# Optimization experiments

Measured on AMD Instinct MI355X. Metric: run time of the kernel, lower is better.

Reference implementation:

```python
import jax, jax.numpy as jnp
import numpy as np

B, LT, LI, DT, DI, D, H = 128, 96, 64, 1024, 2048, 1024, 4
NEG = -2.0 ** 31  # tf.pow(-2.0, 31)
EPS = 1e-3        # keras LayerNormalization default epsilon


def _mha(q_in, k_in, v_in, q_mask, k_mask, Wq, Wk, Wv, Wo):
    # tf split-heads: chunk i of axis 2 -> head i; reshape (B,L,H,d) matches.
    d = D // H
    b = q_in.shape[0]
    q = (q_in @ Wq).reshape(b, -1, H, d)
    k = (k_in @ Wk).reshape(b, -1, H, d)
    v = (v_in @ Wv).reshape(b, -1, H, d)
    scores = jnp.einsum('bqhd,bkhd->bhqk', q, k) / jnp.sqrt(jnp.float32(d))
    mask = (q_mask != 0)[:, None, :, None] & (k_mask != 0)[:, None, None, :]  # [B,1,Lq,Lk]
    scores = jnp.where(mask, scores, NEG)
    attn = jax.nn.softmax(scores, axis=-1)
    attn = jnp.where(mask, attn, 0.0)  # dropout rate is 0.0 -> identity
    out = jnp.einsum('bhqk,bkhd->bqhd', attn, v).reshape(b, -1, D)
    return out @ Wo


def _ln(x, g, b):
    m = jnp.mean(x, axis=-1, keepdims=True)
    v = jnp.var(x, axis=-1, keepdims=True)
    return (x - m) / jnp.sqrt(v + EPS) * g + b


def setup_inputs() -> dict:
    key = jax.random.key(0)
    ks = iter(jax.random.split(key, 40))
    s = 0.02
    inp = {
        'text_embedding': jax.random.normal(next(ks), (B, LT, DT), jnp.float32),
        'image_embedding': jax.random.normal(next(ks), (B, LI, DI), jnp.float32),
        'text_mask': jax.random.randint(next(ks), (B, LT), 0, 2, jnp.int32),
        'image_mask': jax.random.randint(next(ks), (B, LI), 0, 2, jnp.int32),
        'W_tp': jax.random.normal(next(ks), (DT, D), jnp.float32) * s,
        'b_tp': jnp.zeros((D,), jnp.float32),
        'W_ip': jax.random.normal(next(ks), (DI, D), jnp.float32) * s,
        'b_ip': jnp.zeros((D,), jnp.float32),
        # text cross-attn (query=image_proj, key=text_proj, value=RAW text)
        'ta_Wq': jax.random.normal(next(ks), (D, D), jnp.float32) * s,
        'ta_Wk': jax.random.normal(next(ks), (D, D), jnp.float32) * s,
        'ta_Wv': jax.random.normal(next(ks), (DT, D), jnp.float32) * s,
        'ta_Wo': jax.random.normal(next(ks), (D, D), jnp.float32) * s,
        # image cross-attn (query=text_proj, key=image_proj, value=RAW image)
        'ia_Wq': jax.random.normal(next(ks), (D, D), jnp.float32) * s,
        'ia_Wk': jax.random.normal(next(ks), (D, D), jnp.float32) * s,
        'ia_Wv': jax.random.normal(next(ks), (DI, D), jnp.float32) * s,
        'ia_Wo': jax.random.normal(next(ks), (D, D), jnp.float32) * s,
        # self-attention blocks
        'ts_Wq': jax.random.normal(next(ks), (D, D), jnp.float32) * s,
        'ts_Wk': jax.random.normal(next(ks), (D, D), jnp.float32) * s,
        'ts_Wv': jax.random.normal(next(ks), (D, D), jnp.float32) * s,
        'ts_Wo': jax.random.normal(next(ks), (D, D), jnp.float32) * s,
        'is_Wq': jax.random.normal(next(ks), (D, D), jnp.float32) * s,
        'is_Wk': jax.random.normal(next(ks), (D, D), jnp.float32) * s,
        'is_Wv': jax.random.normal(next(ks), (D, D), jnp.float32) * s,
        'is_Wo': jax.random.normal(next(ks), (D, D), jnp.float32) * s,
        # layernorm params
        'ln_ta_g': jnp.ones((D,), jnp.float32), 'ln_ta_b': jnp.zeros((D,), jnp.float32),
        'ln_ia_g': jnp.ones((D,), jnp.float32), 'ln_ia_b': jnp.zeros((D,), jnp.float32),
        'ln_ts_g': jnp.ones((D,), jnp.float32), 'ln_ts_b': jnp.zeros((D,), jnp.float32),
        'ln_is_g': jnp.ones((D,), jnp.float32), 'ln_is_b': jnp.zeros((D,), jnp.float32),
    }
    return inp


def reference(text_embedding, image_embedding, text_mask, image_mask,
              W_tp, b_tp, W_ip, b_ip,
              ta_Wq, ta_Wk, ta_Wv, ta_Wo,
              ia_Wq, ia_Wk, ia_Wv, ia_Wo,
              ts_Wq, ts_Wk, ts_Wv, ts_Wo,
              is_Wq, is_Wk, is_Wv, is_Wo,
              ln_ta_g, ln_ta_b, ln_ia_g, ln_ia_b,
              ln_ts_g, ln_ts_b, ln_is_g, ln_is_b):
    text_proj = text_embedding @ W_tp + b_tp    # [B,LT,D]
    image_proj = image_embedding @ W_ip + b_ip  # [B,LI,D]
    # cross attention (note asymmetric query/key masks, raw-value inputs)
    text_att = _mha(image_proj, text_proj, text_embedding, image_mask, text_mask,
                    ta_Wq, ta_Wk, ta_Wv, ta_Wo)   # [B,LI,D]
    image_att = _mha(text_proj, image_proj, image_embedding, text_mask, image_mask,
                     ia_Wq, ia_Wk, ia_Wv, ia_Wo)  # [B,LT,D]
    text_att = _ln(text_att, ln_ta_g, ln_ta_b)
    image_att = _ln(image_att, ln_ia_g, ln_ia_b)
    # self attention
    text_att = _mha(text_att, text_att, text_att, image_mask, image_mask,
                    ts_Wq, ts_Wk, ts_Wv, ts_Wo)
    image_att = _mha(image_att, image_att, image_att, text_mask, text_mask,
                     is_Wq, is_Wk, is_Wv, is_Wo)
    text_att = _ln(text_att, ln_ts_g, ln_ts_b)
    image_att = _ln(image_att, ln_is_g, ln_is_b)
    return (text_att, image_att)
```

## Files before the change

### kernel.cpp

```cpp
#include <hip/hip_runtime.h>

typedef __bf16 bf16_t;
typedef __attribute__((ext_vector_type(8))) __bf16 bf16x8;
typedef __attribute__((ext_vector_type(4))) __bf16 bf16x4;
typedef __attribute__((ext_vector_type(4))) float f32x4;

__device__ __forceinline__ void async_copy16(const bf16_t* g, bf16_t* l) {
    __builtin_amdgcn_global_load_lds(
        (const __attribute__((address_space(1))) void*)g,
        (__attribute__((address_space(3))) void*)l, 16, 0, 0);
}

__global__ __launch_bounds__(256) void cvt_bf16(const float* __restrict__ in,
                                                bf16_t* __restrict__ out) {
    int i = (blockIdx.x * 256 + threadIdx.x) * 4;
    float4 v = *(const float4*)(in + i);
    bf16x4 o;
    o[0] = (__bf16)v.x; o[1] = (__bf16)v.y; o[2] = (__bf16)v.z; o[3] = (__bf16)v.w;
    *(bf16x4*)(out + i) = o;
}

__global__ __launch_bounds__(256) void transpose_group(const float* __restrict__ s0,
                                                       const float* __restrict__ s1,
                                                       const float* __restrict__ s2,
                                                       bf16_t* __restrict__ dst, int K) {
    const float* in;
    if (blockIdx.z == 0) in = s0;
    else if (blockIdx.z == 1) in = s1;
    else in = s2;
    bf16_t* out = dst + (size_t)blockIdx.z * 1024 * K;
    __shared__ float tile[32][33];
    int t = threadIdx.x;
    int tx = t & 31, ty = t >> 5;
    int n0 = blockIdx.x * 32, k0 = blockIdx.y * 32;
#pragma unroll
    for (int i = 0; i < 4; i++) {
        int k = k0 + ty + i * 8;
        tile[ty + i * 8][tx] = in[(size_t)k * 1024 + n0 + tx];
    }
    __syncthreads();
#pragma unroll
    for (int i = 0; i < 4; i++) {
        int n = n0 + ty + i * 8;
        out[(size_t)n * K + k0 + tx] = (bf16_t)tile[tx][ty + i * 8];
    }
}

__global__ __launch_bounds__(256) void fuse_bias(const float* __restrict__ src,
                                                 float* __restrict__ out) {
    int i = blockIdx.x * 256 + threadIdx.x;
    out[i] = (i < 1024) ? src[i] : 0.f;
}

__global__ __launch_bounds__(512, 2) void gemm256(const bf16_t* __restrict__ A,
                                                  const bf16_t* __restrict__ Bt,
                                                  const float* __restrict__ bias,
                                                  bf16_t* __restrict__ o0,
                                                  bf16_t* __restrict__ o1,
                                                  bf16_t* __restrict__ o2,
                                                  int M, int N, int K) {
    (void)M; (void)N;
    __shared__ bf16_t Ls[65536];
    const int t = threadIdx.x;
    const int w = t >> 6, lane = t & 63;
    const int l16 = lane & 15, quad = lane >> 4;
    const int wm2 = w >> 2, wn4 = w & 3;

    const int nx = gridDim.x;
    const int nwg = nx * gridDim.y;
    const int flat = blockIdx.y * nx + blockIdx.x;
    const int chunk = nwg >> 3;
    const int swz = (flat & 7) * chunk + (flat >> 3);
    const int bm = (swz % nx) * 256;
    const int bn = (swz / nx) * 256;

    const int NT = K >> 5;

    const int sl = t & 7;
    const int pl = (t >> 3) & 63;
    const int ss = sl ^ (pl & 7);
    const int srow = (pl << 1) | (ss >> 2);
    const int scol = (ss & 3) << 3;
    const bf16_t* gA = A + (size_t)(bm + srow) * K + scol;
    const bf16_t* gB = Bt + (size_t)(bn + srow) * K + scol;
    const size_t rstep = (size_t)128 * K;
    const int ldW = w * 512;

    int offA[8], offB[4];
#pragma unroll
    for (int mf = 0; mf < 8; mf++) {
        int row = wm2 * 128 + mf * 16 + l16;
        int p = row >> 1;
        int s2 = (((row & 1) << 2) | quad) ^ (p & 7);
        offA[mf] = p * 64 + s2 * 8;
    }
#pragma unroll
    for (int nf = 0; nf < 4; nf++) {
        int row = wn4 * 64 + nf * 16 + l16;
        int p = row >> 1;
        int s2 = (((row & 1) << 2) | quad) ^ (p & 7);
        offB[nf] = 8192 + p * 64 + s2 * 8;
    }

    const f32x4 zero = {0.f, 0.f, 0.f, 0.f};
    f32x4 acc[8][4];
#pragma unroll
    for (int i = 0; i < 8; i++)
#pragma unroll
        for (int j = 0; j < 4; j++) acc[i][j] = zero;

#pragma unroll
    for (int pt = 0; pt < 3; pt++) {
        bf16_t* lb = Ls + pt * 16384 + ldW;
        const bf16_t* a0 = gA + pt * 32;
        const bf16_t* b0 = gB + pt * 32;
        async_copy16(a0, lb);
        async_copy16(a0 + rstep, lb + 4096);
        async_copy16(b0, lb + 8192);
        async_copy16(b0 + rstep, lb + 12288);
    }
    asm volatile("s_waitcnt vmcnt(8)" ::: "memory");
    __builtin_amdgcn_s_barrier();
    __builtin_amdgcn_sched_barrier(0);

    for (int t0 = 0; t0 < NT; t0++) {
        const bf16_t* cb = Ls + (t0 & 3) * 16384;
        bf16_t* sb = Ls + ((t0 + 3) & 3) * 16384 + ldW;
        const bf16_t* ga = gA + (size_t)(t0 + 3) * 32;
        const bf16_t* gb = gB + (size_t)(t0 + 3) * 32;
        const bool st = (t0 + 3 < NT);
        bf16x8 bq[4], aq[4], ar[4];

#pragma unroll
        for (int nf = 0; nf < 4; nf++) bq[nf] = *(const bf16x8*)(cb + offB[nf]);
#pragma unroll
        for (int mf = 0; mf < 4; mf++) aq[mf] = *(const bf16x8*)(cb + offA[mf]);
        if (st) {
            async_copy16(ga, sb);
            async_copy16(ga + rstep, sb + 4096);
        }
        __builtin_amdgcn_s_barrier();
        __builtin_amdgcn_s_setprio(1);
#pragma unroll
        for (int mf = 0; mf < 4; mf++)
#pragma unroll
            for (int nf = 0; nf < 4; nf++)
                acc[mf][nf] = __builtin_amdgcn_mfma_f32_16x16x32_bf16(aq[mf], bq[nf], acc[mf][nf], 0, 0, 0);
        __builtin_amdgcn_s_setprio(0);
        __builtin_amdgcn_s_barrier();

#pragma unroll
        for (int mf = 0; mf < 4; mf++) ar[mf] = *(const bf16x8*)(cb + offA[4 + mf]);
        if (st) {
            async_copy16(gb, sb + 8192);
            async_copy16(gb + rstep, sb + 12288);
        }
        __builtin_amdgcn_s_barrier();
        __builtin_amdgcn_s_setprio(1);
#pragma unroll
        for (int mf = 0; mf < 4; mf++)
#pragma unroll
            for (int nf = 0; nf < 4; nf++)
                acc[4 + mf][nf] = __builtin_amdgcn_mfma_f32_16x16x32_bf16(ar[mf], bq[nf], acc[4 + mf][nf], 0, 0, 0);
        __builtin_amdgcn_s_setprio(0);

        if (t0 + 1 < NT) {
            if (t0 + 3 < NT)      asm volatile("s_waitcnt vmcnt(8)" ::: "memory");
            else if (t0 + 2 < NT) asm volatile("s_waitcnt vmcnt(4)" ::: "memory");
            else                  asm volatile("s_waitcnt vmcnt(0)" ::: "memory");
            __builtin_amdgcn_s_barrier();
            __builtin_amdgcn_sched_barrier(0);
        }
    }

    bf16_t* outp;
    if (bn < 1024) outp = o0;
    else if (bn < 2048) outp = o1;
    else outp = o2;
    const int cseg = bn & 1023;
    float bsv[4];
#pragma unroll
    for (int nf = 0; nf < 4; nf++)
        bsv[nf] = bias ? bias[bn + wn4 * 64 + nf * 16 + l16] : 0.f;
#pragma unroll
    for (int mf = 0; mf < 8; mf++) {
        int r0 = bm + wm2 * 128 + mf * 16 + quad * 4;
#pragma unroll
        for (int nf = 0; nf < 4; nf++) {
            int c = cseg + wn4 * 64 + nf * 16 + l16;
#pragma unroll
            for (int r = 0; r < 4; r++)
                outp[(size_t)(r0 + r) * 1024 + c] = (bf16_t)(acc[mf][nf][r] + bsv[nf]);
        }
    }
}

template <int LQ, int LK>
__global__ __launch_bounds__(256) void attn_kernel(const bf16_t* __restrict__ Q,
                                                   const bf16_t* __restrict__ Kb,
                                                   const bf16_t* __restrict__ V,
                                                   const int* __restrict__ qmask,
                                                   const int* __restrict__ kmask,
                                                   bf16_t* __restrict__ O) {
    constexpr int VSTR = LK + 8;
    constexpr int NQT = LQ / 16, NKT = LK / 16, NKB = LK / 32;
    __shared__ bf16_t Vt[256 * VSTR];
    __shared__ bf16_t Pb[4 * 16 * LK];

    const int t = threadIdx.x;
    const int w = t >> 6, lane = t & 63;
    const int quad = lane >> 4, l16 = lane & 15;
    const int b = blockIdx.x >> 2;
    const int h = blockIdx.x & 3;
    const int hoff = h * 256;

    for (int idx = t; idx < LK * 32; idx += 256) {
        int k = idx % LK;
        int e0 = (idx / LK) * 8;
        bf16x8 v = *(const bf16x8*)(V + (size_t)(b * LK + k) * 1024 + hoff + e0);
#pragma unroll
        for (int j = 0; j < 8; j++) Vt[(e0 + j) * VSTR + k] = v[j];
    }
    __syncthreads();

    bf16_t* P = Pb + w * (16 * LK);

    for (int qt = w; qt < NQT; qt += 4) {
        const int qrow = b * LQ + qt * 16;
        bf16x8 qf[8];
#pragma unroll
        for (int kb = 0; kb < 8; kb++)
            qf[kb] = *(const bf16x8*)(Q + (size_t)(qrow + l16) * 1024 + hoff + kb * 32 + quad * 8);

        f32x4 s[NKT];
        const f32x4 zero = {0.f, 0.f, 0.f, 0.f};
#pragma unroll
        for (int nt = 0; nt < NKT; nt++) {
            f32x4 a = zero;
#pragma unroll
            for (int kb = 0; kb < 8; kb++) {
                bf16x8 kf = *(const bf16x8*)(Kb + (size_t)(b * LK + nt * 16 + l16) * 1024 + hoff + kb * 32 + quad * 8);
                a = __builtin_amdgcn_mfma_f32_16x16x32_bf16(qf[kb], kf, a, 0, 0, 0);
            }
            s[nt] = a;
        }

        int km[NKT];
#pragma unroll
        for (int nt = 0; nt < NKT; nt++) km[nt] = kmask[b * LK + nt * 16 + l16];
        int qmv[4];
#pragma unroll
        for (int r = 0; r < 4; r++) qmv[r] = qmask[b * LQ + qt * 16 + quad * 4 + r];

        float rmax[4], rsum[4];
#pragma unroll
        for (int r = 0; r < 4; r++) rmax[r] = -3.0e38f;
#pragma unroll
        for (int nt = 0; nt < NKT; nt++)
#pragma unroll
            for (int r = 0; r < 4; r++) {
                float v = s[nt][r] * 0.0625f;
                bool ok = (qmv[r] != 0) && (km[nt] != 0);
                s[nt][r] = ok ? v : -3.0e38f;
                rmax[r] = fmaxf(rmax[r], s[nt][r]);
            }
#pragma unroll
        for (int r = 0; r < 4; r++)
            for (int off = 1; off < 16; off <<= 1)
                rmax[r] = fmaxf(rmax[r], __shfl_xor(rmax[r], off, 16));
#pragma unroll
        for (int r = 0; r < 4; r++) rsum[r] = 0.f;
#pragma unroll
        for (int nt = 0; nt < NKT; nt++)
#pragma unroll
            for (int r = 0; r < 4; r++) {
                float p = (s[nt][r] > -1.0e38f) ? __expf(s[nt][r] - rmax[r]) : 0.f;
                s[nt][r] = p;
                rsum[r] += p;
            }
#pragma unroll
        for (int r = 0; r < 4; r++)
            for (int off = 1; off < 16; off <<= 1)
                rsum[r] += __shfl_xor(rsum[r], off, 16);
#pragma unroll
        for (int r = 0; r < 4; r++) rsum[r] = (rsum[r] > 0.f) ? 1.f / rsum[r] : 0.f;

#pragma unroll
        for (int nt = 0; nt < NKT; nt++)
#pragma unroll
            for (int r = 0; r < 4; r++)
                P[(quad * 4 + r) * LK + nt * 16 + l16] = (bf16_t)(s[nt][r] * rsum[r]);
        asm volatile("s_waitcnt lgkmcnt(0)" ::: "memory");

        bf16x8 pf[NKB];
#pragma unroll
        for (int kb = 0; kb < NKB; kb++)
            pf[kb] = *(const bf16x8*)(P + l16 * LK + kb * 32 + quad * 8);

#pragma unroll
        for (int et = 0; et < 16; et++) {
            f32x4 o = zero;
#pragma unroll
            for (int kb = 0; kb < NKB; kb++) {
                bf16x8 vf = *(const bf16x8*)(Vt + (et * 16 + l16) * VSTR + kb * 32 + quad * 8);
                o = __builtin_amdgcn_mfma_f32_16x16x32_bf16(pf[kb], vf, o, 0, 0, 0);
            }
#pragma unroll
            for (int r = 0; r < 4; r++)
                O[(size_t)(qrow + quad * 4 + r) * 1024 + hoff + et * 16 + l16] = (bf16_t)o[r];
        }
    }
}

__global__ __launch_bounds__(256) void ln_kernel(const bf16_t* __restrict__ in,
                                                 const float* __restrict__ g,
                                                 const float* __restrict__ be,
                                                 float* __restrict__ outF,
                                                 bf16_t* __restrict__ outB) {
    __shared__ float red[8];
    const int row = blockIdx.x, t = threadIdx.x;
    bf16x4 xb = *(const bf16x4*)(in + (size_t)row * 1024 + t * 4);
    float x0 = (float)xb[0], x1 = (float)xb[1], x2 = (float)xb[2], x3 = (float)xb[3];
    float s = x0 + x1 + x2 + x3;
    float ss = x0 * x0 + x1 * x1 + x2 * x2 + x3 * x3;
    for (int off = 1; off < 64; off <<= 1) {
        s += __shfl_xor(s, off);
        ss += __shfl_xor(ss, off);
    }
    int w = t >> 6, lane = t & 63;
    if (lane == 0) { red[w * 2] = s; red[w * 2 + 1] = ss; }
    __syncthreads();
    if (t == 0) {
        float a = 0.f, b2 = 0.f;
        for (int i = 0; i < 4; i++) { a += red[i * 2]; b2 += red[i * 2 + 1]; }
        red[0] = a; red[1] = b2;
    }
    __syncthreads();
    float mean = red[0] * (1.f / 1024.f);
    float var = red[1] * (1.f / 1024.f) - mean * mean;
    float rstd = rsqrtf(var + 1e-3f);
    float4 gv = *(const float4*)(g + t * 4);
    float4 bv = *(const float4*)(be + t * 4);
    float y0 = (x0 - mean) * rstd * gv.x + bv.x;
    float y1 = (x1 - mean) * rstd * gv.y + bv.y;
    float y2 = (x2 - mean) * rstd * gv.z + bv.z;
    float y3 = (x3 - mean) * rstd * gv.w + bv.w;
    if (outF) {
        float4 o = {y0, y1, y2, y3};
        *(float4*)(outF + (size_t)row * 1024 + t * 4) = o;
    }
    if (outB) {
        bf16x4 o;
        o[0] = (__bf16)y0; o[1] = (__bf16)y1; o[2] = (__bf16)y2; o[3] = (__bf16)y3;
        *(bf16x4*)(outB + (size_t)row * 1024 + t * 4) = o;
    }
}

extern "C" void kernel_launch(void* const* d_in, const int* in_sizes, int n_in,
                              void* d_out, int out_size, void* d_ws, size_t ws_size,
                              hipStream_t stream) {
    (void)in_sizes; (void)n_in; (void)out_size; (void)ws_size;
    const float* tE = (const float*)d_in[0];
    const float* iE = (const float*)d_in[1];
    const int* tMask = (const int*)d_in[2];
    const int* iMask = (const int*)d_in[3];

    const size_t MB = 1048576;
    char* ws = (char*)d_ws;
    bf16_t* WB = (bf16_t*)ws;
    float* biasT = (float*)(ws + 8 * MB);
    float* biasI = biasT + 2048;
    char* AB = ws + 9 * MB;
    auto buf = [&](int mb) { return (bf16_t*)(AB + (size_t)mb * MB); };

    auto TG = [&](int i0, int i1, int i2, int parts, int K) {
        transpose_group<<<dim3(32, K / 32, parts), 256, 0, stream>>>(
            (const float*)d_in[i0], i1 >= 0 ? (const float*)d_in[i1] : (const float*)d_in[i0],
            i2 >= 0 ? (const float*)d_in[i2] : (const float*)d_in[i0], WB, K);
    };
    auto gemm = [&](const bf16_t* A, const float* bias, bf16_t* out0, bf16_t* out1,
                    bf16_t* out2, int M, int N, int K) {
        gemm256<<<dim3(M / 256, N / 256), 512, 0, stream>>>(A, WB, bias, out0, out1, out2, M, N, K);
    };

    fuse_bias<<<8, 256, 0, stream>>>((const float*)d_in[5], biasT);
    fuse_bias<<<8, 256, 0, stream>>>((const float*)d_in[7], biasI);

    cvt_bf16<<<12288, 256, 0, stream>>>(tE, buf(88));
    TG(4, 10, -1, 2, 1024);
    gemm(buf(88), biasT, buf(32), buf(64), nullptr, 12288, 2048, 1024);
    cvt_bf16<<<16384, 256, 0, stream>>>(iE, buf(88));
    TG(6, 14, -1, 2, 2048);
    gemm(buf(88), biasI, buf(0), buf(16), nullptr, 8192, 2048, 2048);
    TG(9, 12, -1, 2, 1024);
    gemm(buf(32), nullptr, buf(88), buf(112), nullptr, 12288, 2048, 1024);
    TG(8, 13, -1, 2, 1024);
    gemm(buf(0), nullptr, buf(32), buf(48), nullptr, 8192, 2048, 1024);
    attn_kernel<64, 96><<<512, 256, 0, stream>>>(buf(32), buf(88), buf(64), iMask, tMask, buf(0));
    attn_kernel<96, 64><<<512, 256, 0, stream>>>(buf(112), buf(48), buf(16), tMask, iMask, buf(64));
    TG(11, -1, -1, 1, 1024);
    gemm(buf(0), nullptr, buf(32), nullptr, nullptr, 8192, 1024, 1024);
    ln_kernel<<<8192, 256, 0, stream>>>(buf(32), (const float*)d_in[24], (const float*)d_in[25], nullptr, buf(88));
    TG(15, -1, -1, 1, 1024);
    gemm(buf(64), nullptr, buf(0), nullptr, nullptr, 12288, 1024, 1024);
    ln_kernel<<<12288, 256, 0, stream>>>(buf(0), (const float*)d_in[26], (const float*)d_in[27], nullptr, buf(104));
    TG(16, 17, 18, 3, 1024);
    gemm(buf(88), nullptr, buf(0), buf(16), buf(32), 8192, 3072, 1024);
    attn_kernel<64, 64><<<512, 256, 0, stream>>>(buf(0), buf(16), buf(32), iMask, iMask, buf(48));
    TG(19, -1, -1, 1, 1024);
    gemm(buf(48), nullptr, buf(64), nullptr, nullptr, 8192, 1024, 1024);
    ln_kernel<<<8192, 256, 0, stream>>>(buf(64), (const float*)d_in[28], (const float*)d_in[29], (float*)d_out, nullptr);
    TG(20, 21, 22, 3, 1024);
    gemm(buf(104), nullptr, buf(0), buf(24), buf(48), 12288, 3072, 1024);
    attn_kernel<96, 96><<<512, 256, 0, stream>>>(buf(0), buf(24), buf(48), tMask, tMask, buf(72));
    TG(23, -1, -1, 1, 1024);
    gemm(buf(72), nullptr, buf(96), nullptr, nullptr, 12288, 1024, 1024);
    ln_kernel<<<12288, 256, 0, stream>>>(buf(96), (const float*)d_in[30], (const float*)d_in[31],
                                         (float*)d_out + 8388608, nullptr);
}
```

Before: 998.3 us.

## Shrink GEMM tile to 256x128 with 4 waves and triple-buffered LDS

Switches the bf16 GEMM from 256x256 tiles with 8 waves and a 4-stage LDS ring to 256x128 tiles with 4 waves and a 3-stage ring. This roughly halves LDS per block (about 72KB instead of 128KB), so more blocks can be resident per CU, and it doubles the grid for better CU fill. Each wave still computes a 128x64 sub-tile. The trade-off is lower arithmetic intensity per block, since each A tile is reloaded across twice as many N blocks, and a shallower prefetch depth.

```diff
diff --git a/kernel.cpp b/kernel.cpp
--- a/kernel.cpp
+++ b/kernel.cpp
@@ -52,7 +52,7 @@
     out[i] = (i < 1024) ? src[i] : 0.f;
 }
 
-__global__ __launch_bounds__(512, 2) void gemm256(const bf16_t* __restrict__ A,
+__global__ __launch_bounds__(256, 2) void gemm256(const bf16_t* __restrict__ A,
                                                   const bf16_t* __restrict__ Bt,
                                                   const float* __restrict__ bias,
                                                   bf16_t* __restrict__ o0,
@@ -60,11 +60,11 @@
                                                   bf16_t* __restrict__ o2,
                                                   int M, int N, int K) {
     (void)M; (void)N;
-    __shared__ bf16_t Ls[65536];
+    __shared__ bf16_t Ls[36864];
     const int t = threadIdx.x;
     const int w = t >> 6, lane = t & 63;
     const int l16 = lane & 15, quad = lane >> 4;
-    const int wm2 = w >> 2, wn4 = w & 3;
+    const int wm = (w >> 1) * 128, wn = (w & 1) * 64;
 
     const int nx = gridDim.x;
     const int nwg = nx * gridDim.y;
@@ -72,34 +72,48 @@
     const int chunk = nwg >> 3;
     const int swz = (flat & 7) * chunk + (flat >> 3);
     const int bm = (swz % nx) * 256;
-    const int bn = (swz / nx) * 256;
+    const int bn = (swz / nx) * 128;
 
     const int NT = K >> 5;
 
     const int sl = t & 7;
-    const int pl = (t >> 3) & 63;
-    const int ss = sl ^ (pl & 7);
-    const int srow = (pl << 1) | (ss >> 2);
+    const int pl8 = t >> 3;
+    const int ss = sl ^ (pl8 & 7);
+    const int srow = (pl8 << 1) | (ss >> 2);
     const int scol = (ss & 3) << 3;
-    const bf16_t* gA = A + (size_t)(bm + srow) * K + scol;
-    const bf16_t* gB = Bt + (size_t)(bn + srow) * K + scol;
-    const size_t rstep = (size_t)128 * K;
+    const bf16_t* pA = A + (size_t)(bm + srow) * K + scol;
+    const bf16_t* pB = Bt + (size_t)(bn + srow) * K + scol;
     const int ldW = w * 512;
 
+    auto stageA = [&](int tt, int bi) {
+        bf16_t* d = Ls + bi * 8192 + ldW;
+        const bf16_t* s = pA + (size_t)tt * 32;
+        async_copy16(s, d);
+        async_copy16(s + (size_t)64 * K, d + 2048);
+        async_copy16(s + (size_t)128 * K, d + 4096);
+        async_copy16(s + (size_t)192 * K, d + 6144);
+    };
+    auto stageB = [&](int tt, int bi) {
+        bf16_t* d = Ls + 24576 + bi * 4096 + ldW;
+        const bf16_t* s = pB + (size_t)tt * 32;
+        async_copy16(s, d);
+        async_copy16(s + (size_t)64 * K, d + 2048);
+    };
+
     int offA[8], offB[4];
 #pragma unroll
     for (int mf = 0; mf < 8; mf++) {
-        int row = wm2 * 128 + mf * 16 + l16;
+        int row = wm + mf * 16 + l16;
         int p = row >> 1;
         int s2 = (((row & 1) << 2) | quad) ^ (p & 7);
         offA[mf] = p * 64 + s2 * 8;
     }
 #pragma unroll
     for (int nf = 0; nf < 4; nf++) {
-        int row = wn4 * 64 + nf * 16 + l16;
+        int row = wn + nf * 16 + l16;
         int p = row >> 1;
         int s2 = (((row & 1) << 2) | quad) ^ (p & 7);
-        offB[nf] = 8192 + p * 64 + s2 * 8;
+        offB[nf] = p * 64 + s2 * 8;
     }
 
     const f32x4 zero = {0.f, 0.f, 0.f, 0.f};
@@ -109,36 +123,26 @@
 #pragma unroll
         for (int j = 0; j < 4; j++) acc[i][j] = zero;
 
-#pragma unroll
-    for (int pt = 0; pt < 3; pt++) {
-        bf16_t* lb = Ls + pt * 16384 + ldW;
-        const bf16_t* a0 = gA + pt * 32;
-        const bf16_t* b0 = gB + pt * 32;
-        async_copy16(a0, lb);
-        async_copy16(a0 + rstep, lb + 4096);
-        async_copy16(b0, lb + 8192);
-        async_copy16(b0 + rstep, lb + 12288);
-    }
-    asm volatile("s_waitcnt vmcnt(8)" ::: "memory");
+    stageA(0, 0); stageB(0, 0);
+    stageA(1, 1); stageB(1, 1);
+    asm volatile("s_waitcnt vmcnt(6)" ::: "memory");
     __builtin_amdgcn_s_barrier();
     __builtin_amdgcn_sched_barrier(0);
 
-    for (int t0 = 0; t0 < NT; t0++) {
-        const bf16_t* cb = Ls + (t0 & 3) * 16384;
-        bf16_t* sb = Ls + ((t0 + 3) & 3) * 16384 + ldW;
-        const bf16_t* ga = gA + (size_t)(t0 + 3) * 32;
-        const bf16_t* gb = gB + (size_t)(t0 + 3) * 32;
-        const bool st = (t0 + 3 < NT);
+    int ri = 0;
+    for (int t0 = 0; t0 < NT; ++t0) {
+        const bf16_t* ca = Ls + ri * 8192;
+        const bf16_t* cbv = Ls + 24576 + ri * 4096;
+        const int si = (ri >= 1) ? ri - 1 : 2;
+        const bool st2 = (t0 + 2 < NT);
+
+        if (st2) stageA(t0 + 2, si);
         bf16x8 bq[4], aq[4], ar[4];
-
-#pragma unroll
-        for (int nf = 0; nf < 4; nf++) bq[nf] = *(const bf16x8*)(cb + offB[nf]);
-#pragma unroll
-        for (int mf = 0; mf < 4; mf++) aq[mf] = *(const bf16x8*)(cb + offA[mf]);
-        if (st) {
-            async_copy16(ga, sb);
-            async_copy16(ga + rstep, sb + 4096);
-        }
+#pragma unroll
+        for (int nf = 0; nf < 4; nf++) bq[nf] = *(const bf16x8*)(cbv + offB[nf]);
+#pragma unroll
+        for (int mf = 0; mf < 4; mf++) aq[mf] = *(const bf16x8*)(ca + offA[mf]);
+        if (st2) stageB(t0 + 2, si);
         __builtin_amdgcn_s_barrier();
         __builtin_amdgcn_s_setprio(1);
 #pragma unroll
@@ -150,11 +154,7 @@
         __builtin_amdgcn_s_barrier();
 
 #pragma unroll
-        for (int mf = 0; mf < 4; mf++) ar[mf] = *(const bf16x8*)(cb + offA[4 + mf]);
-        if (st) {
-            async_copy16(gb, sb + 8192);
-            async_copy16(gb + rstep, sb + 12288);
-        }
+        for (int mf = 0; mf < 4; mf++) ar[mf] = *(const bf16x8*)(ca + offA[4 + mf]);
         __builtin_amdgcn_s_barrier();
         __builtin_amdgcn_s_setprio(1);
 #pragma unroll
@@ -165,12 +165,12 @@
         __builtin_amdgcn_s_setprio(0);
 
         if (t0 + 1 < NT) {
-            if (t0 + 3 < NT)      asm volatile("s_waitcnt vmcnt(8)" ::: "memory");
-            else if (t0 + 2 < NT) asm volatile("s_waitcnt vmcnt(4)" ::: "memory");
-            else                  asm volatile("s_waitcnt vmcnt(0)" ::: "memory");
+            if (st2) asm volatile("s_waitcnt vmcnt(6)" ::: "memory");
+            else     asm volatile("s_waitcnt vmcnt(0)" ::: "memory");
             __builtin_amdgcn_s_barrier();
             __builtin_amdgcn_sched_barrier(0);
         }
+        ri = (ri == 2) ? 0 : ri + 1;
     }
 
     bf16_t* outp;
@@ -181,13 +181,13 @@
     float bsv[4];
 #pragma unroll
     for (int nf = 0; nf < 4; nf++)
-        bsv[nf] = bias ? bias[bn + wn4 * 64 + nf * 16 + l16] : 0.f;
+        bsv[nf] = bias ? bias[bn + wn + nf * 16 + l16] : 0.f;
 #pragma unroll
     for (int mf = 0; mf < 8; mf++) {
-        int r0 = bm + wm2 * 128 + mf * 16 + quad * 4;
+        int r0 = bm + wm + mf * 16 + quad * 4;
 #pragma unroll
         for (int nf = 0; nf < 4; nf++) {
-            int c = cseg + wn4 * 64 + nf * 16 + l16;
+            int c = cseg + wn + nf * 16 + l16;
 #pragma unroll
             for (int r = 0; r < 4; r++)
                 outp[(size_t)(r0 + r) * 1024 + c] = (bf16_t)(acc[mf][nf][r] + bsv[nf]);
@@ -380,7 +380,7 @@
     };
     auto gemm = [&](const bf16_t* A, const float* bias, bf16_t* out0, bf16_t* out1,
                     bf16_t* out2, int M, int N, int K) {
-        gemm256<<<dim3(M / 256, N / 256), 512, 0, stream>>>(A, WB, bias, out0, out1, out2, M, N, K);
+        gemm256<<<dim3(M / 256, N / 128), 256, 0, stream>>>(A, WB, bias, out0, out1, out2, M, N, K);
     };
 
     fuse_bias<<<8, 256, 0, stream>>>((const float*)d_in[5], biasT);
```

New measurement: 1.003 ms. About the same (+0.5%).
